# Kernel optimization log

Hardware: AMD Instinct MI355X
Metric: run time of the kernel (lower is better)

The kernel has to match this reference:

```python
import jax, jax.numpy as jnp
import numpy as np
from jax import lax

DIM = 128
DIM_PREV = 64
DIM_NEXT = 256
HEADS = 4
HID = int(DIM * 2.66)  # 340
B, H, W = 8, 128, 128


def conv2d(x, w, stride=1, pad=0, groups=1):
    return lax.conv_general_dilated(
        x, w, (stride, stride), ((pad, pad), (pad, pad)),
        feature_group_count=groups,
        dimension_numbers=('NCHW', 'OIHW', 'NCHW'))


def layernorm_c(x, w, b):
    # WithBias LayerNorm over channel dim (unbiased=False var), eps=1e-5
    mu = x.mean(axis=1, keepdims=True)
    var = ((x - mu) ** 2).mean(axis=1, keepdims=True)
    return (x - mu) / jnp.sqrt(var + 1e-5) * w[None, :, None, None] + b[None, :, None, None]


def pixel_shuffle(x, r=2):
    b, c, h, w = x.shape
    co = c // (r * r)
    return x.reshape(b, co, r, r, h, w).transpose(0, 1, 4, 2, 5, 3).reshape(b, co, h * r, w * r)


def attention(x, temperature, qkv_w, qkv_dw_w, proj_w, heads):
    b, c, h, w = x.shape
    qkv = conv2d(conv2d(x, qkv_w), qkv_dw_w, pad=1, groups=3 * c)
    q, k, v = jnp.split(qkv, 3, axis=1)
    rs = lambda t: t.reshape(b, heads, c // heads, h * w)
    q, k, v = rs(q), rs(k), rs(v)
    q = q / jnp.maximum(jnp.linalg.norm(q, axis=-1, keepdims=True), 1e-12)
    k = k / jnp.maximum(jnp.linalg.norm(k, axis=-1, keepdims=True), 1e-12)
    # channel-wise attention: [b, heads, c/h, c/h]
    attn = jax.nn.softmax(jnp.einsum('bhcn,bhdn->bhcd', q, k) * temperature[None], axis=-1)
    out = jnp.einsum('bhcd,bhdn->bhcn', attn, v).reshape(b, c, h, w)
    return conv2d(out, proj_w)


def ffn(x, pin_w, dw_w, pout_w):
    x = conv2d(x, pin_w)
    x = conv2d(x, dw_w, pad=1, groups=x.shape[1])
    x1, x2 = jnp.split(x, 2, axis=1)
    return conv2d(jax.nn.gelu(x1, approximate=False) * x2, pout_w)


def setup_inputs() -> dict:
    key = jax.random.key(0)
    ks = jax.random.split(key, 16)
    s = 0.05
    return {
        'x_main': jax.random.normal(ks[0], (B, DIM, H, W), jnp.float32),
        'x_prev': jax.random.normal(ks[1], (B, DIM_PREV, 2 * H, 2 * W), jnp.float32),
        'x_next': jax.random.normal(ks[2], (B, DIM_NEXT, H // 2, W // 2), jnp.float32),
        'alpha_down': jnp.float32(0.5),
        'alpha_up': jnp.float32(0.5),
        'down_w': jax.random.normal(ks[3], (DIM, DIM_PREV, 3, 3), jnp.float32) * s,
        'up_w': jax.random.normal(ks[4], (DIM * 4, DIM_NEXT, 1, 1), jnp.float32) * s,
        'norm1_w': jnp.ones((DIM,), jnp.float32),
        'norm1_b': jnp.zeros((DIM,), jnp.float32),
        'temperature': jnp.ones((HEADS, 1, 1), jnp.float32),
        'qkv_w': jax.random.normal(ks[5], (3 * DIM, DIM, 1, 1), jnp.float32) * s,
        'qkv_dw_w': jax.random.normal(ks[6], (3 * DIM, 1, 3, 3), jnp.float32) * s,
        'proj_w': jax.random.normal(ks[7], (DIM, DIM, 1, 1), jnp.float32) * s,
        'norm2_w': jnp.ones((DIM,), jnp.float32),
        'norm2_b': jnp.zeros((DIM,), jnp.float32),
        'ffn_in_w': jax.random.normal(ks[8], (2 * HID, DIM, 1, 1), jnp.float32) * s,
        'ffn_dw_w': jax.random.normal(ks[9], (2 * HID, 1, 3, 3), jnp.float32) * s,
        'ffn_out_w': jax.random.normal(ks[10], (DIM, HID, 1, 1), jnp.float32) * s,
    }


def reference(x_main, x_prev, x_next, alpha_down, alpha_up, down_w, up_w,
              norm1_w, norm1_b, temperature, qkv_w, qkv_dw_w, proj_w,
              norm2_w, norm2_b, ffn_in_w, ffn_dw_w, ffn_out_w):
    f = x_main + alpha_down * conv2d(x_prev, down_w, stride=2, pad=1)
    f = f + alpha_up * pixel_shuffle(conv2d(x_next, up_w))
    x = attention(layernorm_c(f, norm1_w, norm1_b), temperature, qkv_w, qkv_dw_w, proj_w, HEADS)
    x = x_main + x
    x = x + ffn(layernorm_c(x, norm2_w, norm2_b), ffn_in_w, ffn_dw_w, ffn_out_w)
    return x
```

## Files before the change

kernel.cpp:

```cpp
#include <hip/hip_runtime.h>
#include <hip/hip_bf16.h>
#include <math.h>

using bf16 = __hip_bfloat16;
#define DEV static __device__ __forceinline__

typedef float  fx4   __attribute__((ext_vector_type(4)));
typedef short  s16x8 __attribute__((ext_vector_type(8)));
typedef short  s16x4 __attribute__((ext_vector_type(4)));
typedef __bf16 bfx8  __attribute__((ext_vector_type(8)));

constexpr int BATCH = 8;
constexpr int CDIM  = 128;
constexpr int NPIX  = 16384;
constexpr int HIDF  = 340;
constexpr int KFF   = 352;
constexpr int MFI   = 768;

DEV float uu2f(unsigned short u) { return __uint_as_float(((unsigned)u) << 16); }
DEV unsigned short f2us(float f) { bf16 h = __float2bfloat16(f); return *(unsigned short*)&h; }
DEV float bl2f(bf16 v) { return __bfloat162float(v); }

constexpr size_t OFF_SL1   = 0;
constexpr size_t OFF_XNEXT = OFF_SL1;
constexpr size_t OFF_UP    = OFF_SL1 + 16777216;
constexpr size_t OFF_XPREV = OFF_SL1 + 50331648;
constexpr size_t SZ_SL1    = 178257920;
constexpr size_t OFF_SL2   = OFF_SL1 + SZ_SL1;
constexpr size_t OFF_SL3   = OFF_SL2 + 100663296;
constexpr size_t OFF_SL4   = OFF_SL3 + 33554432;
constexpr size_t OFF_SL5   = OFF_SL4 + 33554432;
constexpr size_t OFF_W     = OFF_SL5 + 33554432;
constexpr size_t OFF_WUP   = OFF_W;
constexpr size_t OFF_WQKV  = OFF_W +  262144;
constexpr size_t OFF_WPRJ  = OFF_W +  360448;
constexpr size_t OFF_WFIN  = OFF_W +  393216;
constexpr size_t OFF_WFOUT = OFF_W +  589824;
constexpr size_t OFF_WTAP  = OFF_W +  679936;
constexpr size_t OFF_ZP    = OFF_W +  827392;
constexpr size_t OFF_NBUF  = OFF_W +  974848;
constexpr size_t OFF_S     = OFF_W +  983040;

__global__ void conv_pad(const float* __restrict__ src, bf16* __restrict__ dst,
                         int Rs, int Cs, int Rd, int Cd)
{
    int n = Rd * Cd;
    for (int i = blockIdx.x * 256 + threadIdx.x; i < n; i += gridDim.x * 256) {
        int r = i / Cd, c = i % Cd;
        dst[i] = (r < Rs && c < Cs) ? __float2bfloat16(src[r * Cs + c]) : bf16(0.f);
    }
}

__global__ void wtap_prep(const float* __restrict__ src, bf16* __restrict__ dst)
{
    int i = blockIdx.x * 256 + threadIdx.x;
    if (i >= 9 * 128 * 64) return;
    int tap = i >> 13, rm = i & 8191, co = rm >> 6, ci = rm & 63;
    dst[i] = __float2bfloat16(src[(co * 64 + ci) * 9 + tap]);
}

__global__ __launch_bounds__(256) void transpose_c2p(
    const float* __restrict__ in, bf16* __restrict__ out, int C, int HW)
{
    __shared__ float ts[32][33];
    int hw0 = blockIdx.x * 32, c0 = blockIdx.y * 32, b = blockIdx.z;
    int rl = threadIdx.x >> 5, cl = threadIdx.x & 31;
#pragma unroll
    for (int i = 0; i < 4; i++)
        ts[rl + i * 8][cl] = in[((size_t)b * C + c0 + rl + i * 8) * HW + hw0 + cl];
    __syncthreads();
#pragma unroll
    for (int i = 0; i < 4; i++)
        out[((size_t)b * HW + hw0 + rl + i * 8) * C + c0 + cl] =
            __float2bfloat16(ts[cl][rl + i * 8]);
}

template <int EPI>
__global__ __launch_bounds__(256) void gemm_mfma(
    const bf16* __restrict__ Act, const bf16* __restrict__ Wt,
    int K, int Npb, int Mtrue, int Mstride,
    bf16* __restrict__ outB,
    const float* __restrict__ xmain, bf16* __restrict__ x_out,
    const float* __restrict__ nw, const float* __restrict__ nb,
    const bf16* __restrict__ xres, float* __restrict__ outF)
{
    __shared__ short As[128 * 32];
    __shared__ short Bs[128 * 32];
    const int t = threadIdx.x;
    const int w = t >> 6, lane = t & 63;
    const int wr = w >> 1, wc = w & 1;
    const int lr = lane & 15, lg = lane >> 4;
    const int n0 = blockIdx.x * 128;
    const int m0 = blockIdx.y * 128;
    const int b  = blockIdx.z;
    const bf16* Abase = Act + (size_t)b * Npb * K;

    fx4 acc[4][4];
#pragma unroll
    for (int i = 0; i < 4; i++)
#pragma unroll
        for (int j = 0; j < 4; j++) acc[i][j] = fx4{0.f, 0.f, 0.f, 0.f};

    const int f0 = w * 128 + lane, f1 = f0 + 64;
    const int r0 = f0 >> 2, c0 = (f0 & 3) * 8;
    const int r1 = f1 >> 2, c1 = (f1 & 3) * 8;

    for (int ks = 0; ks < K; ks += 32) {
        __builtin_amdgcn_global_load_lds(
            (const __attribute__((address_space(1))) void*)(Abase + (size_t)(n0 + r0) * K + ks + c0),
            (__attribute__((address_space(3))) void*)(As + w * 1024), 16, 0, 0);
        __builtin_amdgcn_global_load_lds(
            (const __attribute__((address_space(1))) void*)(Abase + (size_t)(n0 + r1) * K + ks + c1),
            (__attribute__((address_space(3))) void*)(As + w * 1024 + 512), 16, 0, 0);
        __builtin_amdgcn_global_load_lds(
            (const __attribute__((address_space(1))) void*)(Wt + (size_t)(m0 + r0) * K + ks + c0),
            (__attribute__((address_space(3))) void*)(Bs + w * 1024), 16, 0, 0);
        __builtin_amdgcn_global_load_lds(
            (const __attribute__((address_space(1))) void*)(Wt + (size_t)(m0 + r1) * K + ks + c1),
            (__attribute__((address_space(3))) void*)(Bs + w * 1024 + 512), 16, 0, 0);
        __syncthreads();
        bfx8 af[4], bw[4];
#pragma unroll
        for (int mi = 0; mi < 4; mi++)
            af[mi] = __builtin_bit_cast(bfx8,
                *(const s16x8*)&As[(wr * 64 + mi * 16 + lr) * 32 + lg * 8]);
#pragma unroll
        for (int ni = 0; ni < 4; ni++)
            bw[ni] = __builtin_bit_cast(bfx8,
                *(const s16x8*)&Bs[(wc * 64 + ni * 16 + lr) * 32 + lg * 8]);
#pragma unroll
        for (int mi = 0; mi < 4; mi++)
#pragma unroll
            for (int ni = 0; ni < 4; ni++)
                acc[mi][ni] = __builtin_amdgcn_mfma_f32_16x16x32_bf16(
                    af[mi], bw[ni], acc[mi][ni], 0, 0, 0);
        __syncthreads();
    }

    if (EPI == 0) {
#pragma unroll
        for (int mi = 0; mi < 4; mi++)
#pragma unroll
            for (int ni = 0; ni < 4; ni++) {
                int co = m0 + wc * 64 + ni * 16 + lr;
                if (co < Mtrue) {
#pragma unroll
                    for (int r = 0; r < 4; r++) {
                        int px = n0 + wr * 64 + mi * 16 + lg * 4 + r;
                        outB[((size_t)b * Npb + px) * Mstride + co] =
                            __float2bfloat16(acc[mi][ni][r]);
                    }
                }
            }
    } else if (EPI == 1) {
        float xv[4][4][4];
#pragma unroll
        for (int mi = 0; mi < 4; mi++)
#pragma unroll
            for (int ni = 0; ni < 4; ni++) {
                int co = wc * 64 + ni * 16 + lr;
                fx4 x4 = *(const fx4*)&xmain[((size_t)b * 128 + co) * 16384 +
                                             n0 + wr * 64 + mi * 16 + lg * 4];
#pragma unroll
                for (int r = 0; r < 4; r++) xv[mi][ni][r] = x4[r] + acc[mi][ni][r];
            }
        __shared__ float ps[2][128];
        __shared__ float pss[2][128];
#pragma unroll
        for (int mi = 0; mi < 4; mi++)
#pragma unroll
            for (int r = 0; r < 4; r++) {
                float s = 0.f, s2 = 0.f;
#pragma unroll
                for (int ni = 0; ni < 4; ni++) {
                    float v = xv[mi][ni][r]; s += v; s2 += v * v;
                }
#pragma unroll
                for (int m = 1; m < 16; m <<= 1) {
                    s  += __shfl_xor(s, m);
                    s2 += __shfl_xor(s2, m);
                }
                if (lr == 0) {
                    int row = wr * 64 + mi * 16 + lg * 4 + r;
                    ps[wc][row] = s; pss[wc][row] = s2;
                }
            }
        __syncthreads();
        float nwv[4], nbv[4];
#pragma unroll
        for (int ni = 0; ni < 4; ni++) {
            int co = wc * 64 + ni * 16 + lr;
            nwv[ni] = nw[co]; nbv[ni] = nb[co];
        }
#pragma unroll
        for (int mi = 0; mi < 4; mi++)
#pragma unroll
            for (int r = 0; r < 4; r++) {
                int row = wr * 64 + mi * 16 + lg * 4 + r;
                float s  = ps[0][row] + ps[1][row];
                float s2 = pss[0][row] + pss[1][row];
                float mu = s * (1.f / 128.f);
                float var = s2 * (1.f / 128.f) - mu * mu;
                float rstd = rsqrtf(var + 1e-5f);
                size_t px = (size_t)b * 16384 + n0 + row;
#pragma unroll
                for (int ni = 0; ni < 4; ni++) {
                    int co = wc * 64 + ni * 16 + lr;
                    float v = xv[mi][ni][r];
                    x_out[px * 128 + co] = __float2bfloat16(v);
                    outB[px * 128 + co] = __float2bfloat16((v - mu) * rstd * nwv[ni] + nbv[ni]);
                }
            }
    } else {
#pragma unroll
        for (int mi = 0; mi < 4; mi++)
#pragma unroll
            for (int ni = 0; ni < 4; ni++) {
                int co = wc * 64 + ni * 16 + lr;
                int pxb = n0 + wr * 64 + mi * 16 + lg * 4;
                fx4 o;
#pragma unroll
                for (int r = 0; r < 4; r++)
                    o[r] = acc[mi][ni][r] +
                           bl2f(xres[((size_t)b * 16384 + pxb + r) * 128 + co]);
                *(fx4*)&outF[((size_t)b * 128 + co) * 16384 + pxb] = o;
            }
    }
}

__global__ __launch_bounds__(256) void down_mfma_ln(
    const bf16* __restrict__ xprev_pm,
    const float* __restrict__ xmain,
    const bf16* __restrict__ up_pm,
    const bf16* __restrict__ wtap,
    const float* __restrict__ alpha_d, const float* __restrict__ alpha_u,
    const float* __restrict__ n1w, const float* __restrict__ n1b,
    const bf16* __restrict__ zeropage,
    bf16* __restrict__ y1)
{
    __shared__ short As[128 * 64];
    __shared__ short Bs[128 * 64];
    __shared__ float ps[2][128];
    __shared__ float pss[2][128];
    const int t = threadIdx.x;
    const int w = t >> 6, lane = t & 63;
    const int wr = w >> 1, wc = w & 1;
    const int lr = lane & 15, lg = lane >> 4;
    const int y = blockIdx.x;
    const int b = blockIdx.y;

    const int srow0 = 32 * w + (lane >> 3);
    const int sci8  = lane & 7;
    const short* wtbase = (const short*)wtap;

    fx4 acc[4][4];
#pragma unroll
    for (int i = 0; i < 4; i++)
#pragma unroll
        for (int j = 0; j < 4; j++) acc[i][j] = fx4{0.f, 0.f, 0.f, 0.f};

#pragma unroll
    for (int tap = 0; tap < 9; tap++) {
        const int dy = tap / 3, dx = tap % 3;
        const int iy = 2 * y - 1 + dy;
        const bool rowok = (iy >= 0) && (iy < 256);
        const short* arow = (const short*)xprev_pm +
                            (((size_t)b * 65536 + (size_t)iy * 256) * 64);
#pragma unroll
        for (int i = 0; i < 4; i++) {
            int row = srow0 + 8 * i;
            int ix = 2 * row - 1 + dx;
            const short* src = (rowok && ix >= 0 && ix < 256)
                                 ? (arow + (size_t)ix * 64 + sci8 * 8)
                                 : (const short*)zeropage;
            __builtin_amdgcn_global_load_lds(
                (const __attribute__((address_space(1))) void*)src,
                (__attribute__((address_space(3))) void*)(As + w * 2048 + i * 512), 16, 0, 0);
            __builtin_amdgcn_global_load_lds(
                (const __attribute__((address_space(1))) void*)
                    (wtbase + tap * 8192 + w * 2048 + i * 512 + lane * 8),
                (__attribute__((address_space(3))) void*)(Bs + w * 2048 + i * 512), 16, 0, 0);
        }
        __syncthreads();
        bfx8 af[4][2], bw[4][2];
#pragma unroll
        for (int mi = 0; mi < 4; mi++)
#pragma unroll
            for (int ks = 0; ks < 2; ks++)
                af[mi][ks] = __builtin_bit_cast(bfx8,
                    *(const s16x8*)&As[(wr * 64 + mi * 16 + lr) * 64 + ks * 32 + lg * 8]);
#pragma unroll
        for (int ni = 0; ni < 4; ni++)
#pragma unroll
            for (int ks = 0; ks < 2; ks++)
                bw[ni][ks] = __builtin_bit_cast(bfx8,
                    *(const s16x8*)&Bs[(wc * 64 + ni * 16 + lr) * 64 + ks * 32 + lg * 8]);
#pragma unroll
        for (int mi = 0; mi < 4; mi++)
#pragma unroll
            for (int ni = 0; ni < 4; ni++)
#pragma unroll
                for (int ks = 0; ks < 2; ks++)
                    acc[mi][ni] = __builtin_amdgcn_mfma_f32_16x16x32_bf16(
                        af[mi][ks], bw[ni][ks], acc[mi][ni], 0, 0, 0);
        __syncthreads();
    }

    const float ad = alpha_d[0], au = alpha_u[0];
    const int n2base = (y >> 1) * 64;
    const int chb2 = (y & 1) * 2;
    float fv[4][4][4];
#pragma unroll
    for (int mi = 0; mi < 4; mi++) {
        const int x0 = wr * 64 + mi * 16 + lg * 4;
#pragma unroll
        for (int ni = 0; ni < 4; ni++) {
            const int co = wc * 64 + ni * 16 + lr;
            fx4 xm = *(const fx4*)&xmain[(((size_t)b * 128 + co) * 128 + y) * 128 + x0];
            const short* uprow = (const short*)up_pm +
                ((size_t)b * 4096 + n2base + (x0 >> 1)) * 512 + co * 4 + chb2;
            unsigned up01 = *(const unsigned*)uprow;
            unsigned up23 = *(const unsigned*)(uprow + 512);
            fv[mi][ni][0] = xm[0] + ad * acc[mi][ni][0] + au * uu2f((unsigned short)(up01 & 0xffff));
            fv[mi][ni][1] = xm[1] + ad * acc[mi][ni][1] + au * uu2f((unsigned short)(up01 >> 16));
            fv[mi][ni][2] = xm[2] + ad * acc[mi][ni][2] + au * uu2f((unsigned short)(up23 & 0xffff));
            fv[mi][ni][3] = xm[3] + ad * acc[mi][ni][3] + au * uu2f((unsigned short)(up23 >> 16));
        }
    }
#pragma unroll
    for (int mi = 0; mi < 4; mi++)
#pragma unroll
        for (int r = 0; r < 4; r++) {
            float s = 0.f, s2 = 0.f;
#pragma unroll
            for (int ni = 0; ni < 4; ni++) {
                float v = fv[mi][ni][r]; s += v; s2 += v * v;
            }
#pragma unroll
            for (int m = 1; m < 16; m <<= 1) {
                s  += __shfl_xor(s, m);
                s2 += __shfl_xor(s2, m);
            }
            if (lr == 0) {
                int row = wr * 64 + mi * 16 + lg * 4 + r;
                ps[wc][row] = s; pss[wc][row] = s2;
            }
        }
    __syncthreads();
    float nwv[4], nbv[4];
#pragma unroll
    for (int ni = 0; ni < 4; ni++) {
        int co = wc * 64 + ni * 16 + lr;
        nwv[ni] = n1w[co]; nbv[ni] = n1b[co];
    }
#pragma unroll
    for (int mi = 0; mi < 4; mi++)
#pragma unroll
        for (int r = 0; r < 4; r++) {
            int row = wr * 64 + mi * 16 + lg * 4 + r;
            float s  = ps[0][row] + ps[1][row];
            float s2 = pss[0][row] + pss[1][row];
            float mu = s * (1.f / 128.f);
            float var = s2 * (1.f / 128.f) - mu * mu;
            float rstd = rsqrtf(var + 1e-5f);
            size_t px = (size_t)b * 16384 + (size_t)y * 128 + row;
#pragma unroll
            for (int ni = 0; ni < 4; ni++) {
                int co = wc * 64 + ni * 16 + lr;
                ((short*)y1)[px * 128 + co] =
                    (short)f2us((fv[mi][ni][r] - mu) * rstd * nwv[ni] + nbv[ni]);
            }
        }
}

__global__ __launch_bounds__(256) void dw_qkv(
    const bf16* __restrict__ in, const float* __restrict__ w, bf16* __restrict__ out)
{
    __shared__ short ins[6 * 34 * 40];
    const int t = threadIdx.x;
    const int cg = blockIdx.y, b = blockIdx.z;
    const int x0 = (blockIdx.x & 3) * 32, y0 = (blockIdx.x >> 2) * 4;
    for (int g = t; g < 816; g += 256) {
        int r = g / 136, rm = g % 136, xx = rm >> 2, c8 = rm & 3;
        int gy = y0 - 1 + r, gx = x0 - 1 + xx;
        s16x8 v = s16x8{0,0,0,0,0,0,0,0};
        if (gy >= 0 && gy < 128 && gx >= 0 && gx < 128)
            v = *(const s16x8*)((const short*)in +
                  ((size_t)(b << 14) + (gy << 7) + gx) * 384 + cg * 32 + c8 * 8);
        *(s16x8*)&ins[(r * 34 + xx) * 40 + c8 * 8] = v;
    }
    __syncthreads();
    const int x = t >> 3, cq = t & 7, cl = cq * 4, ch = cg * 32 + cl;
    float wv[4][9];
#pragma unroll
    for (int cc = 0; cc < 4; cc++)
#pragma unroll
        for (int k = 0; k < 9; k++) wv[cc][k] = w[(ch + cc) * 9 + k];
#pragma unroll
    for (int yy = 0; yy < 4; yy++) {
        fx4 a = fx4{0.f, 0.f, 0.f, 0.f};
#pragma unroll
        for (int dy = 0; dy < 3; dy++)
#pragma unroll
            for (int dx = 0; dx < 3; dx++) {
                s16x4 v = *(const s16x4*)&ins[((yy + dy) * 34 + x + dx) * 40 + cl];
#pragma unroll
                for (int cc = 0; cc < 4; cc++)
                    a[cc] = fmaf(wv[cc][dy * 3 + dx], uu2f((unsigned short)v[cc]), a[cc]);
            }
        s16x4 pk;
#pragma unroll
        for (int cc = 0; cc < 4; cc++) pk[cc] = (short)f2us(a[cc]);
        *(s16x4*)((short*)out + ((size_t)(b << 14) + ((y0 + yy) << 7) + x0 + x) * 384 + ch) = pk;
    }
}

__global__ __launch_bounds__(256) void dw_gate(
    const bf16* __restrict__ h1, const float* __restrict__ w, bf16* __restrict__ g)
{
    __shared__ short in1[6 * 34 * 40];
    __shared__ short in2[6 * 34 * 40];
    const int t = threadIdx.x;
    const int cg = blockIdx.y, b = blockIdx.z;
    const int x0 = (blockIdx.x & 3) * 32, y0 = (blockIdx.x >> 2) * 4;
    for (int gg = t; gg < 1632; gg += 256) {
        int half = gg >= 816;
        int g2 = gg - half * 816;
        int r = g2 / 136, rm = g2 % 136, xx = rm >> 2, c8 = rm & 3;
        int gy = y0 - 1 + r, gx = x0 - 1 + xx;
        int chb = cg * 32 + c8 * 8 + (half ? 340 : 0);
        int lim = half ? 680 : 340;
        s16x8 v = s16x8{0,0,0,0,0,0,0,0};
        if (gy >= 0 && gy < 128 && gx >= 0 && gx < 128) {
            const short* base = (const short*)h1 +
                ((size_t)(b << 14) + (gy << 7) + gx) * 680 + chb;
            if (chb + 8 <= lim) {
                s16x4 lo = *(const s16x4*)base;
                s16x4 hi = *(const s16x4*)(base + 4);
#pragma unroll
                for (int e = 0; e < 4; e++) { v[e] = lo[e]; v[e + 4] = hi[e]; }
            } else {
#pragma unroll
                for (int e = 0; e < 8; e++) v[e] = (chb + e < lim) ? base[e] : (short)0;
            }
        }
        short* dst = half ? in2 : in1;
        *(s16x8*)&dst[(r * 34 + xx) * 40 + c8 * 8] = v;
    }
    __syncthreads();
    const int x = t >> 3, cq = t & 7, cl = cq * 4;
    const int c = cg * 32 + cl;
    float w1[4][9], w2[4][9];
#pragma unroll
    for (int cc = 0; cc < 4; cc++) {
        int cr = c + cc;
        bool ok = cr < 340;
#pragma unroll
        for (int k = 0; k < 9; k++) {
            w1[cc][k] = ok ? w[cr * 9 + k] : 0.f;
            w2[cc][k] = ok ? w[(cr + 340) * 9 + k] : 0.f;
        }
    }
#pragma unroll
    for (int yy = 0; yy < 4; yy++) {
        fx4 a1 = fx4{0.f,0.f,0.f,0.f}, a2 = fx4{0.f,0.f,0.f,0.f};
#pragma unroll
        for (int dy = 0; dy < 3; dy++)
#pragma unroll
            for (int dx = 0; dx < 3; dx++) {
                int off = ((yy + dy) * 34 + x + dx) * 40 + cl;
                s16x4 v1 = *(const s16x4*)&in1[off];
                s16x4 v2 = *(const s16x4*)&in2[off];
#pragma unroll
                for (int cc = 0; cc < 4; cc++) {
                    a1[cc] = fmaf(w1[cc][dy * 3 + dx], uu2f((unsigned short)v1[cc]), a1[cc]);
                    a2[cc] = fmaf(w2[cc][dy * 3 + dx], uu2f((unsigned short)v2[cc]), a2[cc]);
                }
            }
        s16x4 pk;
#pragma unroll
        for (int cc = 0; cc < 4; cc++) {
            float ge = 0.5f * a1[cc] * (1.f + erff(a1[cc] * 0.70710678118f));
            float val = (c + cc < 340) ? ge * a2[cc] : 0.f;
            pk[cc] = (short)f2us(val);
        }
        *(s16x4*)((short*)g + ((size_t)(b << 14) + ((y0 + yy) << 7) + x0 + x) * 352 + c) = pk;
    }
}

__global__ __launch_bounds__(256) void rownorm(const bf16* __restrict__ qkv,
                                               float* __restrict__ nbuf)
{
    int b = blockIdx.x >> 5, chk = blockIdx.x & 31, c = threadIdx.x;
    const short* base = (const short*)qkv + ((size_t)(b * 16384 + chk * 512)) * 384 + c;
    float ss = 0.f;
#pragma unroll 4
    for (int i = 0; i < 512; i++) {
        float v = uu2f((unsigned short)base[(size_t)i * 384]);
        ss = fmaf(v, v, ss);
    }
    atomicAdd(&nbuf[b * 256 + c], ss);
}

__global__ __launch_bounds__(256) void scores(const bf16* __restrict__ qkv,
                                              float* __restrict__ S)
{
    __shared__ short qs[256 * 40];
    __shared__ short ks2[256 * 40];
    const int t = threadIdx.x;
    const int bh = blockIdx.x, b = bh >> 2, h = bh & 3;
    const int n0 = blockIdx.y * 256;
    {
        const short* src = (const short*)qkv + ((size_t)(b * 16384 + n0 + t)) * 384 + h * 32;
#pragma unroll
        for (int i = 0; i < 4; i++) {
            *(s16x8*)&qs[t * 40 + i * 8]  = *(const s16x8*)(src + i * 8);
            *(s16x8*)&ks2[t * 40 + i * 8] = *(const s16x8*)(src + 128 + i * 8);
        }
    }
    __syncthreads();
    const int i2 = t >> 4, j16 = t & 15;
    float a00 = 0.f, a01 = 0.f, a10 = 0.f, a11 = 0.f;
    for (int n = 0; n < 256; n++) {
        unsigned qq = *(const unsigned*)&qs[n * 40 + i2 * 2];
        unsigned kk = *(const unsigned*)&ks2[n * 40 + j16 * 2];
        float q0 = uu2f((unsigned short)(qq & 0xffff)), q1 = uu2f((unsigned short)(qq >> 16));
        float k0 = uu2f((unsigned short)(kk & 0xffff)), k1 = uu2f((unsigned short)(kk >> 16));
        a00 = fmaf(q0, k0, a00); a01 = fmaf(q0, k1, a01);
        a10 = fmaf(q1, k0, a10); a11 = fmaf(q1, k1, a11);
    }
    float* base = S + (size_t)bh * 1024;
    atomicAdd(&base[(i2 * 2 + 0) * 32 + j16 * 2 + 0], a00);
    atomicAdd(&base[(i2 * 2 + 0) * 32 + j16 * 2 + 1], a01);
    atomicAdd(&base[(i2 * 2 + 1) * 32 + j16 * 2 + 0], a10);
    atomicAdd(&base[(i2 * 2 + 1) * 32 + j16 * 2 + 1], a11);
}

__global__ void softmax_k(float* __restrict__ S, const float* __restrict__ nbuf,
                          const float* __restrict__ temp)
{
    __shared__ float invk[32];
    int bh = blockIdx.x, b = bh >> 2, h = bh & 3, i = threadIdx.x;
    invk[i] = 1.f / fmaxf(sqrtf(nbuf[b * 256 + 128 + h * 32 + i]), 1e-12f);
    __syncthreads();
    float ti = temp[h] / fmaxf(sqrtf(nbuf[b * 256 + h * 32 + i]), 1e-12f);
    float* row = S + (size_t)bh * 1024 + i * 32;
    float vals[32], m = -1e30f;
#pragma unroll
    for (int j = 0; j < 32; j++) { vals[j] = row[j] * ti * invk[j]; m = fmaxf(m, vals[j]); }
    float s = 0.f;
#pragma unroll
    for (int j = 0; j < 32; j++) { vals[j] = expf(vals[j] - m); s += vals[j]; }
    float r = 1.f / s;
#pragma unroll
    for (int j = 0; j < 32; j++) row[j] = vals[j] * r;
}

__global__ __launch_bounds__(256) void attnapply(const bf16* __restrict__ qkv,
                                                 const float* __restrict__ S,
                                                 bf16* __restrict__ atto)
{
    __shared__ float sa[1024];
    const int t = threadIdx.x;
    const int bh = blockIdx.x, b = bh >> 2, h = bh & 3;
    const int n0 = blockIdx.y * 1024;
    for (int i = t; i < 1024; i += 256) sa[i] = S[(size_t)bh * 1024 + i];
    __syncthreads();
#pragma unroll
    for (int pp = 0; pp < 4; pp++) {
        int n = n0 + (t << 2) + pp;
        const short* vs = (const short*)qkv + ((size_t)(b * 16384) + n) * 384 + 256 + h * 32;
        float v[32];
#pragma unroll
        for (int i = 0; i < 4; i++) {
            s16x8 vv = *(const s16x8*)(vs + i * 8);
#pragma unroll
            for (int e = 0; e < 8; e++) v[i * 8 + e] = uu2f((unsigned short)vv[e]);
        }
        short ov[32];
#pragma unroll
        for (int c = 0; c < 32; c++) {
            const fx4* row = (const fx4*)&sa[c * 32];
            float a = 0.f;
#pragma unroll
            for (int d4 = 0; d4 < 8; d4++) {
                fx4 w4 = row[d4];
                a += w4[0] * v[d4 * 4] + w4[1] * v[d4 * 4 + 1] +
                     w4[2] * v[d4 * 4 + 2] + w4[3] * v[d4 * 4 + 3];
            }
            ov[c] = (short)f2us(a);
        }
        short* dst = (short*)atto + ((size_t)(b * 16384) + n) * 128 + h * 32;
#pragma unroll
        for (int i = 0; i < 4; i++) *(s16x8*)(dst + i * 8) = *(s16x8*)&ov[i * 8];
    }
}

extern "C" void kernel_launch(void* const* d_in, const int* in_sizes, int n_in,
                              void* d_out, int out_size, void* d_ws, size_t ws_size,
                              hipStream_t stream)
{
    const float* x_main      = (const float*)d_in[0];
    const float* x_prev      = (const float*)d_in[1];
    const float* x_next      = (const float*)d_in[2];
    const float* alpha_down  = (const float*)d_in[3];
    const float* alpha_up    = (const float*)d_in[4];
    const float* down_w      = (const float*)d_in[5];
    const float* up_w        = (const float*)d_in[6];
    const float* norm1_w     = (const float*)d_in[7];
    const float* norm1_b     = (const float*)d_in[8];
    const float* temperature = (const float*)d_in[9];
    const float* qkv_w       = (const float*)d_in[10];
    const float* qkv_dw_w    = (const float*)d_in[11];
    const float* proj_w      = (const float*)d_in[12];
    const float* norm2_w     = (const float*)d_in[13];
    const float* norm2_b     = (const float*)d_in[14];
    const float* ffn_in_w    = (const float*)d_in[15];
    const float* ffn_dw_w    = (const float*)d_in[16];
    const float* ffn_out_w   = (const float*)d_in[17];
    float* out = (float*)d_out;
    (void)in_sizes; (void)n_in; (void)out_size; (void)ws_size;

    char* ws = (char*)d_ws;
    bf16* xnext_pm = (bf16*)(ws + OFF_XNEXT);
    bf16* up_pm    = (bf16*)(ws + OFF_UP);
    bf16* xprev_pm = (bf16*)(ws + OFF_XPREV);
    bf16* qkv_a    = (bf16*)(ws + OFF_SL1);
    bf16* h1       = (bf16*)(ws + OFF_SL1);
    bf16* qkv_b    = (bf16*)(ws + OFF_SL2);
    bf16* gbuf     = (bf16*)(ws + OFF_SL2);
    bf16* y1       = (bf16*)(ws + OFF_SL3);
    bf16* atto     = (bf16*)(ws + OFF_SL3);
    bf16* x_pm     = (bf16*)(ws + OFF_SL4);
    bf16* y2       = (bf16*)(ws + OFF_SL5);
    bf16* Wup      = (bf16*)(ws + OFF_WUP);
    bf16* Wqkv     = (bf16*)(ws + OFF_WQKV);
    bf16* Wprj     = (bf16*)(ws + OFF_WPRJ);
    bf16* Wfin     = (bf16*)(ws + OFF_WFIN);
    bf16* Wfout    = (bf16*)(ws + OFF_WFOUT);
    bf16* Wtap     = (bf16*)(ws + OFF_WTAP);
    bf16* zpage    = (bf16*)(ws + OFF_ZP);
    float* nbuf    = (float*)(ws + OFF_NBUF);
    float* Sbuf    = (float*)(ws + OFF_S);

    hipMemsetAsync(nbuf, 0, 8192 + 131072, stream);
    hipMemsetAsync(zpage, 0, 256, stream);

    conv_pad<<<dim3(512), 256, 0, stream>>>(up_w, Wup, 512, 256, 512, 256);
    conv_pad<<<dim3(192), 256, 0, stream>>>(qkv_w, Wqkv, 384, 128, 384, 128);
    conv_pad<<<dim3(64), 256, 0, stream>>>(proj_w, Wprj, 128, 128, 128, 128);
    conv_pad<<<dim3(384), 256, 0, stream>>>(ffn_in_w, Wfin, 680, 128, MFI, 128);
    conv_pad<<<dim3(176), 256, 0, stream>>>(ffn_out_w, Wfout, 128, 340, 128, KFF);
    wtap_prep<<<dim3(288), 256, 0, stream>>>(down_w, Wtap);

    transpose_c2p<<<dim3(128, 8, BATCH), 256, 0, stream>>>(x_next, xnext_pm, 256, 4096);
    transpose_c2p<<<dim3(2048, 2, BATCH), 256, 0, stream>>>(x_prev, xprev_pm, 64, 65536);

    gemm_mfma<0><<<dim3(32, 4, BATCH), 256, 0, stream>>>(
        xnext_pm, Wup, 256, 4096, 512, 512, up_pm,
        nullptr, nullptr, nullptr, nullptr, nullptr, nullptr);

    down_mfma_ln<<<dim3(128, BATCH), 256, 0, stream>>>(
        xprev_pm, x_main, up_pm, Wtap, alpha_down, alpha_up, norm1_w, norm1_b,
        zpage, y1);

    gemm_mfma<0><<<dim3(128, 3, BATCH), 256, 0, stream>>>(
        y1, Wqkv, 128, NPIX, 384, 384, qkv_a,
        nullptr, nullptr, nullptr, nullptr, nullptr, nullptr);

    dw_qkv<<<dim3(128, 12, BATCH), 256, 0, stream>>>(qkv_a, qkv_dw_w, qkv_b);

    rownorm<<<dim3(256), 256, 0, stream>>>(qkv_b, nbuf);
    scores<<<dim3(32, 64), 256, 0, stream>>>(qkv_b, Sbuf);
    softmax_k<<<dim3(32), 32, 0, stream>>>(Sbuf, nbuf, temperature);
    attnapply<<<dim3(32, 16), 256, 0, stream>>>(qkv_b, Sbuf, atto);

    gemm_mfma<1><<<dim3(128, 1, BATCH), 256, 0, stream>>>(
        atto, Wprj, 128, NPIX, 128, 128, y2,
        x_main, x_pm, norm2_w, norm2_b, nullptr, nullptr);

    gemm_mfma<0><<<dim3(128, 6, BATCH), 256, 0, stream>>>(
        y2, Wfin, 128, NPIX, 680, 680, h1,
        nullptr, nullptr, nullptr, nullptr, nullptr, nullptr);

    dw_gate<<<dim3(128, 11, BATCH), 256, 0, stream>>>(h1, ffn_dw_w, gbuf);

    gemm_mfma<2><<<dim3(128, 1, BATCH), 256, 0, stream>>>(
        gbuf, Wfout, KFF, NPIX, 128, 128, nullptr,
        nullptr, nullptr, nullptr, nullptr, x_pm, out);
}
```

Before: 692.1 us.

## Fuse q/k norm into depthwise conv, loop M in GEMMs, pad h1 layout

Adds a GEMM variant in which each block keeps its activation tile resident in LDS and loops over all output-channel tiles, so activations are read once instead of once per M tile. The depthwise qkv and gate convolutions are merged into one templated kernel that processes 8 rows per block with packed fx2 math and weights staged in shared memory. The qkv version also accumulates the q/k squared norms, which removes the separate rownorm pass. h1 is stored with a padded, aligned 704-channel stride so the gate kernel can use full vector loads. The exact erf GELU is replaced by a sigmoid-based approximation, which may shift accuracy, and an extra kernel zero-fills the pad columns.

```diff
diff --git a/kernel.cpp b/kernel.cpp
--- a/kernel.cpp
+++ b/kernel.cpp
@@ -5,17 +5,18 @@
 using bf16 = __hip_bfloat16;
 #define DEV static __device__ __forceinline__
 
-typedef float  fx4   __attribute__((ext_vector_type(4)));
-typedef short  s16x8 __attribute__((ext_vector_type(8)));
-typedef short  s16x4 __attribute__((ext_vector_type(4)));
-typedef __bf16 bfx8  __attribute__((ext_vector_type(8)));
+typedef float    fx4   __attribute__((ext_vector_type(4)));
+typedef float    fx2   __attribute__((ext_vector_type(2)));
+typedef short    s16x8 __attribute__((ext_vector_type(8)));
+typedef short    s16x4 __attribute__((ext_vector_type(4)));
+typedef __bf16   bfx8  __attribute__((ext_vector_type(8)));
+typedef unsigned int u32x4 __attribute__((ext_vector_type(4)));
 
 constexpr int BATCH = 8;
-constexpr int CDIM  = 128;
 constexpr int NPIX  = 16384;
-constexpr int HIDF  = 340;
 constexpr int KFF   = 352;
 constexpr int MFI   = 768;
+constexpr int H1S   = 704;
 
 DEV float uu2f(unsigned short u) { return __uint_as_float(((unsigned)u) << 16); }
 DEV unsigned short f2us(float f) { bf16 h = __float2bfloat16(f); return *(unsigned short*)&h; }
@@ -25,7 +26,7 @@
 constexpr size_t OFF_XNEXT = OFF_SL1;
 constexpr size_t OFF_UP    = OFF_SL1 + 16777216;
 constexpr size_t OFF_XPREV = OFF_SL1 + 50331648;
-constexpr size_t SZ_SL1    = 178257920;
+constexpr size_t SZ_SL1    = 184549376;
 constexpr size_t OFF_SL2   = OFF_SL1 + SZ_SL1;
 constexpr size_t OFF_SL3   = OFF_SL2 + 100663296;
 constexpr size_t OFF_SL4   = OFF_SL3 + 33554432;
@@ -57,6 +58,16 @@
     if (i >= 9 * 128 * 64) return;
     int tap = i >> 13, rm = i & 8191, co = rm >> 6, ci = rm & 63;
     dst[i] = __float2bfloat16(src[(co * 64 + ci) * 9 + tap]);
+}
+
+__global__ void h1_padzero(bf16* __restrict__ h1)
+{
+    size_t idx = (size_t)blockIdx.x * 256 + threadIdx.x;
+    if (idx >= (size_t)BATCH * NPIX * 24) return;
+    size_t n = idx / 24;
+    int j = (int)(idx % 24);
+    int col = (j < 12) ? 340 + j : 680 + j;
+    h1[n * H1S + col] = bf16(0.f);
 }
 
 __global__ __launch_bounds__(256) void transpose_c2p(
@@ -228,6 +239,84 @@
     }
 }
 
+template <int REMAP>
+__global__ __launch_bounds__(256) void gemm_mloop(
+    const bf16* __restrict__ Act, const bf16* __restrict__ Wt,
+    int nM, int Mtrue, int Mstride, bf16* __restrict__ outB)
+{
+    __shared__ short As[16384];
+    __shared__ short Bs[16384];
+    const int t = threadIdx.x;
+    const int w = t >> 6, lane = t & 63;
+    const int wr = w >> 1, wc = w & 1;
+    const int lr = lane & 15, lg = lane >> 4;
+    const int n0 = blockIdx.x * 128;
+    const int b  = blockIdx.y;
+    const short* Abase = (const short*)Act + (size_t)b * NPIX * 128;
+
+#pragma unroll
+    for (int i = 0; i < 8; i++) {
+        int chunk = i * 256 + w * 64 + lane;
+        int kb = chunk >> 9, row = (chunk >> 2) & 127, c8 = chunk & 3;
+        __builtin_amdgcn_global_load_lds(
+            (const __attribute__((address_space(1))) void*)
+                (Abase + (size_t)(n0 + row) * 128 + kb * 32 + c8 * 8),
+            (__attribute__((address_space(3))) void*)(As + i * 2048 + w * 512), 16, 0, 0);
+    }
+
+    for (int mt = 0; mt < nM; mt++) {
+#pragma unroll
+        for (int i = 0; i < 8; i++) {
+            int chunk = i * 256 + w * 64 + lane;
+            int kb = chunk >> 9, row = (chunk >> 2) & 127, c8 = chunk & 3;
+            __builtin_amdgcn_global_load_lds(
+                (const __attribute__((address_space(1))) void*)
+                    ((const short*)Wt + (size_t)(mt * 128 + row) * 128 + kb * 32 + c8 * 8),
+                (__attribute__((address_space(3))) void*)(Bs + i * 2048 + w * 512), 16, 0, 0);
+        }
+        __syncthreads();
+        fx4 acc[4][4];
+#pragma unroll
+        for (int i = 0; i < 4; i++)
+#pragma unroll
+            for (int j = 0; j < 4; j++) acc[i][j] = fx4{0.f, 0.f, 0.f, 0.f};
+#pragma unroll
+        for (int ks = 0; ks < 4; ks++) {
+            bfx8 af[4], bw[4];
+#pragma unroll
+            for (int mi = 0; mi < 4; mi++)
+                af[mi] = __builtin_bit_cast(bfx8,
+                    *(const s16x8*)&As[ks * 4096 + (wr * 64 + mi * 16 + lr) * 32 + lg * 8]);
+#pragma unroll
+            for (int ni = 0; ni < 4; ni++)
+                bw[ni] = __builtin_bit_cast(bfx8,
+                    *(const s16x8*)&Bs[ks * 4096 + (wc * 64 + ni * 16 + lr) * 32 + lg * 8]);
+#pragma unroll
+            for (int mi = 0; mi < 4; mi++)
+#pragma unroll
+                for (int ni = 0; ni < 4; ni++)
+                    acc[mi][ni] = __builtin_amdgcn_mfma_f32_16x16x32_bf16(
+                        af[mi], bw[ni], acc[mi][ni], 0, 0, 0);
+        }
+        __syncthreads();
+#pragma unroll
+        for (int mi = 0; mi < 4; mi++)
+#pragma unroll
+            for (int ni = 0; ni < 4; ni++) {
+                int co = mt * 128 + wc * 64 + ni * 16 + lr;
+                if (co < Mtrue) {
+                    int cd = (REMAP && co >= 340) ? co + 12 : co;
+#pragma unroll
+                    for (int r = 0; r < 4; r++) {
+                        int px = n0 + wr * 64 + mi * 16 + lg * 4 + r;
+                        outB[((size_t)b * NPIX + px) * Mstride + cd] =
+                            __float2bfloat16(acc[mi][ni][r]);
+                    }
+                }
+            }
+    }
+}
+
 __global__ __launch_bounds__(256) void down_mfma_ln(
     const bf16* __restrict__ xprev_pm,
     const float* __restrict__ xmain,
@@ -373,133 +462,158 @@
         }
 }
 
-__global__ __launch_bounds__(256) void dw_qkv(
-    const bf16* __restrict__ in, const float* __restrict__ w, bf16* __restrict__ out)
-{
-    __shared__ short ins[6 * 34 * 40];
+DEV void dw_accum(const short* __restrict__ L, const float* __restrict__ swb,
+                  int x, int yh, int lofs, fx2 acc[4][4])
+{
+    fx2 wreg[9][4];
+#pragma unroll
+    for (int tap = 0; tap < 9; tap++)
+#pragma unroll
+        for (int k = 0; k < 4; k++)
+            wreg[tap][k] = *(const fx2*)&swb[tap * 32 + lofs + 2 * k];
+#pragma unroll
+    for (int yy = 0; yy < 4; yy++)
+#pragma unroll
+        for (int k = 0; k < 4; k++) acc[yy][k] = fx2{0.f, 0.f};
+#pragma unroll
+    for (int r = 0; r < 6; r++) {
+        fx2 rv[3][4];
+#pragma unroll
+        for (int dxp = 0; dxp < 3; dxp++) {
+            s16x8 raw = *(const s16x8*)&L[((yh * 4 + r) * 34 + x + dxp) * 40 + lofs];
+            u32x4 u = __builtin_bit_cast(u32x4, raw);
+#pragma unroll
+            for (int k = 0; k < 4; k++)
+                rv[dxp][k] = fx2{__uint_as_float(u[k] << 16),
+                                 __uint_as_float(u[k] & 0xffff0000u)};
+        }
+#pragma unroll
+        for (int yy = 0; yy < 4; yy++) {
+            int dy = r - yy;
+            if (dy < 0 || dy > 2) continue;
+#pragma unroll
+            for (int dx = 0; dx < 3; dx++)
+#pragma unroll
+                for (int k = 0; k < 4; k++)
+                    acc[yy][k] += rv[dx][k] * wreg[dy * 3 + dx][k];
+        }
+    }
+}
+
+template <int GATE, int QKNORM>
+__global__ __launch_bounds__(256) void dw_conv(
+    const bf16* __restrict__ in, const float* __restrict__ w,
+    bf16* __restrict__ out, float* __restrict__ nbuf)
+{
+    constexpr int CHST  = GATE ? 704 : 384;
+    constexpr int CHOST = GATE ? 352 : 384;
+    __shared__ short L1[13600];
+    __shared__ short L2[GATE ? 13600 : 8];
+    __shared__ float sw1[288];
+    __shared__ float sw2[GATE ? 288 : 8];
+    __shared__ float snorm[32];
     const int t = threadIdx.x;
+    const int x = t & 31, chg = (t >> 5) & 3, yh = t >> 7;
     const int cg = blockIdx.y, b = blockIdx.z;
-    const int x0 = (blockIdx.x & 3) * 32, y0 = (blockIdx.x >> 2) * 4;
-    for (int g = t; g < 816; g += 256) {
-        int r = g / 136, rm = g % 136, xx = rm >> 2, c8 = rm & 3;
-        int gy = y0 - 1 + r, gx = x0 - 1 + xx;
-        s16x8 v = s16x8{0,0,0,0,0,0,0,0};
+    const int x0 = (blockIdx.x & 3) * 32, y0 = (blockIdx.x >> 2) * 8;
+
+    if (QKNORM && t < 32) snorm[t] = 0.f;
+    if (GATE) {
+        for (int i = t; i < 288; i += 256) {
+            int c = i & 31, tap = i >> 5;
+            int cr = cg * 32 + c;
+            sw1[i] = (cr < 340) ? w[cr * 9 + tap] : 0.f;
+            sw2[i] = (cr < 340) ? w[(cr + 340) * 9 + tap] : 0.f;
+        }
+    } else {
+        for (int i = t; i < 288; i += 256) {
+            int c = i & 31, tap = i >> 5;
+            sw1[i] = w[(cg * 32 + c) * 9 + tap];
+        }
+    }
+    const short* bin = (const short*)in + (size_t)b * NPIX * CHST + cg * 32;
+    const int NCHK = GATE ? 2720 : 1360;
+    for (int id = t; id < NCHK; id += 256) {
+        int half = 0, idd = id;
+        if (GATE && idd >= 1360) { half = 1; idd -= 1360; }
+        int row = idd / 136, rm = idd % 136, pos = rm >> 2, c8 = rm & 3;
+        int gy = y0 - 1 + row, gx = x0 - 1 + pos;
+        s16x8 v = s16x8{0, 0, 0, 0, 0, 0, 0, 0};
         if (gy >= 0 && gy < 128 && gx >= 0 && gx < 128)
-            v = *(const s16x8*)((const short*)in +
-                  ((size_t)(b << 14) + (gy << 7) + gx) * 384 + cg * 32 + c8 * 8);
-        *(s16x8*)&ins[(r * 34 + xx) * 40 + c8 * 8] = v;
+            v = *(const s16x8*)(bin + ((size_t)(gy << 7) + gx) * CHST + half * 352 + c8 * 8);
+        short* dst = (GATE && half) ? L2 : L1;
+        *(s16x8*)&dst[(row * 34 + pos) * 40 + c8 * 8] = v;
     }
     __syncthreads();
-    const int x = t >> 3, cq = t & 7, cl = cq * 4, ch = cg * 32 + cl;
-    float wv[4][9];
-#pragma unroll
-    for (int cc = 0; cc < 4; cc++)
-#pragma unroll
-        for (int k = 0; k < 9; k++) wv[cc][k] = w[(ch + cc) * 9 + k];
+
+    const int lofs = chg * 8;
+    fx2 a1[4][4];
+    dw_accum(L1, sw1, x, yh, lofs, a1);
+    if (GATE) {
+#pragma unroll
+        for (int yy = 0; yy < 4; yy++)
+#pragma unroll
+            for (int k = 0; k < 4; k++) {
+                fx2 v = a1[yy][k];
+#pragma unroll
+                for (int e = 0; e < 2; e++) {
+                    float xx = v[e];
+                    float x2 = xx * xx;
+                    float mzz = xx * fmaf(-0.1029432f, x2, -2.3022082f);
+                    float un = exp2f(mzz);
+                    v[e] = xx * __builtin_amdgcn_rcpf(1.f + un);
+                }
+                a1[yy][k] = v;
+            }
+        fx2 a2[4][4];
+        dw_accum(L2, sw2, x, yh, lofs, a2);
+#pragma unroll
+        for (int yy = 0; yy < 4; yy++)
+#pragma unroll
+            for (int k = 0; k < 4; k++) a1[yy][k] *= a2[yy][k];
+    }
+
+    if (QKNORM && cg < 8) {
+        fx2 sq[4];
+#pragma unroll
+        for (int k = 0; k < 4; k++) {
+            sq[k] = fx2{0.f, 0.f};
+#pragma unroll
+            for (int yy = 0; yy < 4; yy++) sq[k] += a1[yy][k] * a1[yy][k];
+        }
+#pragma unroll
+        for (int m = 1; m < 32; m <<= 1)
+#pragma unroll
+            for (int k = 0; k < 4; k++) {
+                sq[k][0] += __shfl_xor(sq[k][0], m);
+                sq[k][1] += __shfl_xor(sq[k][1], m);
+            }
+        if (x == 0) {
+#pragma unroll
+            for (int k = 0; k < 4; k++) {
+                atomicAdd(&snorm[chg * 8 + 2 * k],     sq[k][0]);
+                atomicAdd(&snorm[chg * 8 + 2 * k + 1], sq[k][1]);
+            }
+        }
+    }
+
 #pragma unroll
     for (int yy = 0; yy < 4; yy++) {
-        fx4 a = fx4{0.f, 0.f, 0.f, 0.f};
-#pragma unroll
-        for (int dy = 0; dy < 3; dy++)
-#pragma unroll
-            for (int dx = 0; dx < 3; dx++) {
-                s16x4 v = *(const s16x4*)&ins[((yy + dy) * 34 + x + dx) * 40 + cl];
-#pragma unroll
-                for (int cc = 0; cc < 4; cc++)
-                    a[cc] = fmaf(wv[cc][dy * 3 + dx], uu2f((unsigned short)v[cc]), a[cc]);
-            }
-        s16x4 pk;
-#pragma unroll
-        for (int cc = 0; cc < 4; cc++) pk[cc] = (short)f2us(a[cc]);
-        *(s16x4*)((short*)out + ((size_t)(b << 14) + ((y0 + yy) << 7) + x0 + x) * 384 + ch) = pk;
-    }
-}
-
-__global__ __launch_bounds__(256) void dw_gate(
-    const bf16* __restrict__ h1, const float* __restrict__ w, bf16* __restrict__ g)
-{
-    __shared__ short in1[6 * 34 * 40];
-    __shared__ short in2[6 * 34 * 40];
-    const int t = threadIdx.x;
-    const int cg = blockIdx.y, b = blockIdx.z;
-    const int x0 = (blockIdx.x & 3) * 32, y0 = (blockIdx.x >> 2) * 4;
-    for (int gg = t; gg < 1632; gg += 256) {
-        int half = gg >= 816;
-        int g2 = gg - half * 816;
-        int r = g2 / 136, rm = g2 % 136, xx = rm >> 2, c8 = rm & 3;
-        int gy = y0 - 1 + r, gx = x0 - 1 + xx;
-        int chb = cg * 32 + c8 * 8 + (half ? 340 : 0);
-        int lim = half ? 680 : 340;
-        s16x8 v = s16x8{0,0,0,0,0,0,0,0};
-        if (gy >= 0 && gy < 128 && gx >= 0 && gx < 128) {
-            const short* base = (const short*)h1 +
-                ((size_t)(b << 14) + (gy << 7) + gx) * 680 + chb;
-            if (chb + 8 <= lim) {
-                s16x4 lo = *(const s16x4*)base;
-                s16x4 hi = *(const s16x4*)(base + 4);
-#pragma unroll
-                for (int e = 0; e < 4; e++) { v[e] = lo[e]; v[e + 4] = hi[e]; }
-            } else {
-#pragma unroll
-                for (int e = 0; e < 8; e++) v[e] = (chb + e < lim) ? base[e] : (short)0;
-            }
-        }
-        short* dst = half ? in2 : in1;
-        *(s16x8*)&dst[(r * 34 + xx) * 40 + c8 * 8] = v;
-    }
-    __syncthreads();
-    const int x = t >> 3, cq = t & 7, cl = cq * 4;
-    const int c = cg * 32 + cl;
-    float w1[4][9], w2[4][9];
-#pragma unroll
-    for (int cc = 0; cc < 4; cc++) {
-        int cr = c + cc;
-        bool ok = cr < 340;
-#pragma unroll
-        for (int k = 0; k < 9; k++) {
-            w1[cc][k] = ok ? w[cr * 9 + k] : 0.f;
-            w2[cc][k] = ok ? w[(cr + 340) * 9 + k] : 0.f;
-        }
-    }
-#pragma unroll
-    for (int yy = 0; yy < 4; yy++) {
-        fx4 a1 = fx4{0.f,0.f,0.f,0.f}, a2 = fx4{0.f,0.f,0.f,0.f};
-#pragma unroll
-        for (int dy = 0; dy < 3; dy++)
-#pragma unroll
-            for (int dx = 0; dx < 3; dx++) {
-                int off = ((yy + dy) * 34 + x + dx) * 40 + cl;
-                s16x4 v1 = *(const s16x4*)&in1[off];
-                s16x4 v2 = *(const s16x4*)&in2[off];
-#pragma unroll
-                for (int cc = 0; cc < 4; cc++) {
-                    a1[cc] = fmaf(w1[cc][dy * 3 + dx], uu2f((unsigned short)v1[cc]), a1[cc]);
-                    a2[cc] = fmaf(w2[cc][dy * 3 + dx], uu2f((unsigned short)v2[cc]), a2[cc]);
-                }
-            }
-        s16x4 pk;
-#pragma unroll
-        for (int cc = 0; cc < 4; cc++) {
-            float ge = 0.5f * a1[cc] * (1.f + erff(a1[cc] * 0.70710678118f));
-            float val = (c + cc < 340) ? ge * a2[cc] : 0.f;
-            pk[cc] = (short)f2us(val);
-        }
-        *(s16x4*)((short*)g + ((size_t)(b << 14) + ((y0 + yy) << 7) + x0 + x) * 352 + c) = pk;
-    }
-}
-
-__global__ __launch_bounds__(256) void rownorm(const bf16* __restrict__ qkv,
-                                               float* __restrict__ nbuf)
-{
-    int b = blockIdx.x >> 5, chk = blockIdx.x & 31, c = threadIdx.x;
-    const short* base = (const short*)qkv + ((size_t)(b * 16384 + chk * 512)) * 384 + c;
-    float ss = 0.f;
-#pragma unroll 4
-    for (int i = 0; i < 512; i++) {
-        float v = uu2f((unsigned short)base[(size_t)i * 384]);
-        ss = fmaf(v, v, ss);
-    }
-    atomicAdd(&nbuf[b * 256 + c], ss);
+        s16x8 pk;
+#pragma unroll
+        for (int k = 0; k < 4; k++) {
+            pk[2 * k]     = (short)f2us(a1[yy][k][0]);
+            pk[2 * k + 1] = (short)f2us(a1[yy][k][1]);
+        }
+        *(s16x8*)((short*)out + (((size_t)b * NPIX) + ((y0 + yh * 4 + yy) << 7) + x0 + x) * CHOST
+                  + cg * 32 + chg * 8) = pk;
+    }
+
+    if (QKNORM) {
+        __syncthreads();
+        if (cg < 8 && t < 32)
+            atomicAdd(&nbuf[b * 256 + cg * 32 + t], snorm[t]);
+    }
 }
 
 __global__ __launch_bounds__(256) void scores(const bf16* __restrict__ qkv,
@@ -664,13 +778,10 @@
         xprev_pm, x_main, up_pm, Wtap, alpha_down, alpha_up, norm1_w, norm1_b,
         zpage, y1);
 
-    gemm_mfma<0><<<dim3(128, 3, BATCH), 256, 0, stream>>>(
-        y1, Wqkv, 128, NPIX, 384, 384, qkv_a,
-        nullptr, nullptr, nullptr, nullptr, nullptr, nullptr);
-
-    dw_qkv<<<dim3(128, 12, BATCH), 256, 0, stream>>>(qkv_a, qkv_dw_w, qkv_b);
-
-    rownorm<<<dim3(256), 256, 0, stream>>>(qkv_b, nbuf);
+    gemm_mloop<0><<<dim3(128, BATCH), 256, 0, stream>>>(y1, Wqkv, 3, 384, 384, qkv_a);
+
+    dw_conv<0, 1><<<dim3(64, 12, BATCH), 256, 0, stream>>>(qkv_a, qkv_dw_w, qkv_b, nbuf);
+
     scores<<<dim3(32, 64), 256, 0, stream>>>(qkv_b, Sbuf);
     softmax_k<<<dim3(32), 32, 0, stream>>>(Sbuf, nbuf, temperature);
     attnapply<<<dim3(32, 16), 256, 0, stream>>>(qkv_b, Sbuf, atto);
@@ -679,11 +790,10 @@
         atto, Wprj, 128, NPIX, 128, 128, y2,
         x_main, x_pm, norm2_w, norm2_b, nullptr, nullptr);
 
-    gemm_mfma<0><<<dim3(128, 6, BATCH), 256, 0, stream>>>(
-        y2, Wfin, 128, NPIX, 680, 680, h1,
-        nullptr, nullptr, nullptr, nullptr, nullptr, nullptr);
-
-    dw_gate<<<dim3(128, 11, BATCH), 256, 0, stream>>>(h1, ffn_dw_w, gbuf);
+    h1_padzero<<<dim3((BATCH * NPIX * 24 + 255) / 256), 256, 0, stream>>>(h1);
+    gemm_mloop<1><<<dim3(128, BATCH), 256, 0, stream>>>(y2, Wfin, 6, 680, H1S, h1);
+
+    dw_conv<1, 0><<<dim3(64, 11, BATCH), 256, 0, stream>>>(h1, ffn_dw_w, gbuf, nullptr);
 
     gemm_mfma<2><<<dim3(128, 1, BATCH), 256, 0, stream>>>(
         gbuf, Wfout, KFF, NPIX, 128, 128, nullptr,
```

Result: faster. 615.7 us (-11.0%).
